# Kernel tuning notes

Hardware: AMD Instinct MI355X
Metric: run time of the kernel (lower is better)

## Reference

```python
import jax, jax.numpy as jnp
import numpy as np

B, T, C = 4, 2048, 1024  # n_embd == input_size == 1024
H, D = 16, 64            # num_heads, head_size


def setup_inputs() -> dict:
    key = jax.random.key(0)
    ks = jax.random.split(key, 5)
    s_in = (1.0 / C) ** 0.5   # ~Linear default init scale
    s_pr = (1.0 / (H * D)) ** 0.5
    return {
        "x": jax.random.normal(ks[0], (B, T, C), dtype=jnp.float32),
        "wq": jax.random.normal(ks[1], (H, C, D), dtype=jnp.float32) * s_in,
        "wk": jax.random.normal(ks[2], (H, C, D), dtype=jnp.float32) * s_in,
        "wv": jax.random.normal(ks[3], (H, C, D), dtype=jnp.float32) * s_in,
        "w_proj": jax.random.normal(ks[4], (H * D, C), dtype=jnp.float32) * s_pr,
        "b_proj": jnp.zeros((C,), dtype=jnp.float32),
    }


def reference(x, wq, wk, wv, w_proj, b_proj):
    Bb, Tt, Cc = x.shape
    # Batched per-head projections: [B,T,C] x [H,C,D] -> [B,H,T,D]
    q = jnp.einsum("btc,hcd->bhtd", x, wq)
    k = jnp.einsum("btc,hcd->bhtd", x, wk)
    v = jnp.einsum("btc,hcd->bhtd", x, wv)
    # NOTE: original scales by C**-0.5 with C = full embedding dim (quirk preserved)
    scale = Cc ** (-0.5)
    scores = jnp.einsum("bhtd,bhsd->bhts", q, k) * scale  # [B,H,T,T]
    causal = jnp.tril(jnp.ones((Tt, Tt), dtype=bool))
    scores = jnp.where(causal, scores, -jnp.inf)
    wei = jax.nn.softmax(scores, axis=-1)
    out = jnp.einsum("bhts,bhsd->bhtd", wei, v)           # [B,H,T,D]
    out = out.transpose(0, 2, 1, 3).reshape(Bb, Tt, -1)    # concat heads [B,T,H*D]
    return out @ w_proj + b_proj                           # [B,T,C]
```

## Files before the change

### kernel.cpp

```cpp
#include <hip/hip_runtime.h>
#include <stdint.h>


typedef uint32_t u32;
typedef __bf16 bf16x8 __attribute__((ext_vector_type(8)));
typedef __bf16 bf16x4 __attribute__((ext_vector_type(4)));
typedef unsigned short us8 __attribute__((ext_vector_type(8)));
typedef float f32x4 __attribute__((ext_vector_type(4)));

#define EXP2F(x) __builtin_amdgcn_exp2f(x)

static __device__ __forceinline__ unsigned short f2bf(float f) {
  union { float f; u32 i; } cv; cv.f = f;
  u32 x = cv.i;
  u32 r = (x + 0x7fffu + ((x >> 16) & 1u)) >> 16;
  return (unsigned short)r;
}

static __device__ __forceinline__ void gload_lds16(const unsigned short* g, unsigned short* l) {
  __builtin_amdgcn_global_load_lds(
      (__attribute__((address_space(1))) u32*)g,
      (__attribute__((address_space(3))) u32*)l, 16, 0, 0);
}

#define G8_LGKM do { asm volatile("s_waitcnt lgkmcnt(0)" ::: "memory"); \
                     __builtin_amdgcn_sched_barrier(0); } while (0)

__global__ __launch_bounds__(256) void prep(
    const float* __restrict__ x, const float* __restrict__ wq,
    const float* __restrict__ wk, const float* __restrict__ wv,
    const float* __restrict__ wp, unsigned short* __restrict__ x_bf,
    unsigned short* __restrict__ wtq, unsigned short* __restrict__ wtp) {
  __shared__ unsigned short lds[64][66];
  const int b = blockIdx.x, tid = threadIdx.x;
  if (b < 4096) {
    size_t i = (size_t)(b * 256 + tid) * 8u;
    float4 a = *(const float4*)(x + i);
    float4 c = *(const float4*)(x + i + 4);
    us8 v;
    v[0] = f2bf(a.x); v[1] = f2bf(a.y); v[2] = f2bf(a.z); v[3] = f2bf(a.w);
    v[4] = f2bf(c.x); v[5] = f2bf(c.y); v[6] = f2bf(c.z); v[7] = f2bf(c.w);
    *(us8*)(x_bf + i) = v;
    return;
  }
  if (b < 4864) {
    int idx = b - 4096;
    int z = idx >> 8, rem = idx & 255;
    int h = rem >> 4, c0 = (rem & 15) << 6;
    const float* src = (z == 0) ? wq : (z == 1) ? wk : wv;
    unsigned short* d = wtq + ((size_t)z << 20);
    const float* s = src + (size_t)h * 65536u + (size_t)c0 * 64u;
#pragma unroll
    for (int it = 0; it < 16; ++it) {
      int i2 = it * 256 + tid;
      int r = i2 >> 6, dd = i2 & 63;
      lds[dd][r] = f2bf(s[r * 64 + dd]);
    }
    __syncthreads();
#pragma unroll
    for (int it = 0; it < 16; ++it) {
      int i2 = it * 256 + tid;
      int dd = i2 >> 6, r = i2 & 63;
      d[(size_t)(h * 64 + dd) * 1024u + c0 + r] = lds[dd][r];
    }
    return;
  }
  {
    int idx = b - 4864;
    int c0 = (idx >> 4) << 6, r0 = (idx & 15) << 6;
#pragma unroll
    for (int it = 0; it < 16; ++it) {
      int i2 = it * 256 + tid;
      int r = i2 >> 6, cc = i2 & 63;
      lds[cc][r] = f2bf(wp[(size_t)(r0 + r) * 1024u + c0 + cc]);
    }
    __syncthreads();
#pragma unroll
    for (int it = 0; it < 16; ++it) {
      int i2 = it * 256 + tid;
      int cc = i2 >> 6, r = i2 & 63;
      wtp[(size_t)(c0 + cc) * 1024u + r0 + r] = lds[cc][r];
    }
  }
}

__global__ __launch_bounds__(256) void transpose_v(
    const unsigned short* __restrict__ v, unsigned short* __restrict__ vt) {
  __shared__ unsigned short lds[64][66];
  const int tid = threadIdx.x;
  const int bh = blockIdx.y, t0 = blockIdx.x * 64;
  const unsigned short* src = v + ((size_t)(bh >> 4) * 2048 + t0) * 1024u + (bh & 15) * 64;
  unsigned short* dst = vt + (size_t)bh * 131072u + t0;
#pragma unroll
  for (int it = 0; it < 16; ++it) {
    int idx = it * 256 + tid;
    int r = idx >> 6, dd = idx & 63;
    lds[dd][r] = src[(size_t)r * 1024u + dd];
  }
  __syncthreads();
#pragma unroll
  for (int it = 0; it < 16; ++it) {
    int idx = it * 256 + tid;
    int dd = idx >> 6, r = idx & 63;
    dst[(size_t)dd * 2048u + r] = lds[dd][r];
  }
}

static __device__ __forceinline__ void gn_stage(const unsigned short* g,
                                                unsigned short* d, int tid) {
#pragma unroll
  for (int l = 0; l < 2; ++l) {
    int cid = l * 512 + tid;
    int r = cid >> 3, c = cid & 7;
    gload_lds16(g + (size_t)r * 1024 + ((c ^ (r & 7)) << 3), d + cid * 8);
  }
}
static __device__ __forceinline__ void gn_ldA(bf16x8 af[4][2], const unsigned short* As,
                                              int wr, int l15, int lhi) {
#pragma unroll
  for (int mi = 0; mi < 4; ++mi)
#pragma unroll
    for (int ks = 0; ks < 2; ++ks) {
      int row = wr * 64 + mi * 16 + l15;
      af[mi][ks] = *(const bf16x8*)(As + row * 64 + ((((ks << 2) | lhi) ^ (row & 7)) << 3));
    }
}
static __device__ __forceinline__ void gn_ldB(bf16x8 bf[2][2], const unsigned short* Bs,
                                              int wc, int np, int l15, int lhi) {
#pragma unroll
  for (int ni = 0; ni < 2; ++ni)
#pragma unroll
    for (int ks = 0; ks < 2; ++ks) {
      int row = wc * 64 + np * 32 + ni * 16 + l15;
      bf[ni][ks] = *(const bf16x8*)(Bs + row * 64 + ((((ks << 2) | lhi) ^ (row & 7)) << 3));
    }
}
static __device__ __forceinline__ void gn_quad(f32x4 acc[4][4], bf16x8 af[4][2],
                                               bf16x8 bf[2][2], int np) {
#pragma unroll
  for (int ks = 0; ks < 2; ++ks)
#pragma unroll
    for (int mi = 0; mi < 4; ++mi)
#pragma unroll
      for (int ni = 0; ni < 2; ++ni)
        acc[mi][np * 2 + ni] = __builtin_amdgcn_mfma_f32_16x16x32_bf16(
            af[mi][ks], bf[ni][ks], acc[mi][np * 2 + ni], 0, 0, 0);
}

template <int F32OUT>
__global__ __launch_bounds__(512, 2) void gemmN(
    const unsigned short* __restrict__ A, const unsigned short* __restrict__ Bt,
    const float* __restrict__ bias, void* __restrict__ Cv) {
  extern __shared__ __align__(16) unsigned short ldsm[];
  unsigned short* Ab = ldsm;
  unsigned short* Bb = ldsm + 16384;
  const int tid = threadIdx.x, wid = tid >> 6, lane = tid & 63;
  const int l15 = lane & 15, lhi = lane >> 4;
  const int wr = wid >> 2, wc = wid & 3;
  const int bid = blockIdx.x;
  const int mt = ((bid & 7) << 3) | ((bid >> 3) & 7);
  const int nt = bid >> 6;
  const int m0 = mt * 128, n0 = nt * 256;
  const unsigned short* Ag = A + (size_t)m0 * 1024;
  const unsigned short* Bg = Bt + (size_t)n0 * 1024;

  f32x4 acc[4][4] = {};
  bf16x8 af[4][2], b0[2][2], b1[2][2];

  gn_stage(Bg, Bb, tid);
  gn_stage(Bg + 128 * 1024, Bb + 8192, tid);
  gn_stage(Ag, Ab, tid);
  gn_stage(Ag + 64, Ab + 8192, tid);
  asm volatile("s_waitcnt vmcnt(2)" ::: "memory");
  __builtin_amdgcn_s_barrier();

  for (int j = 0; j < 8; ++j) {
    const bool last = (j == 7);
    const int kc = j * 128;
    gn_ldA(af, Ab, wr, l15, lhi);
    gn_ldB(b0, Bb, wc, 0, l15, lhi);
    gn_stage(Bg + (kc + 64), Bb + 16384, tid);
    gn_stage(Bg + 128 * 1024 + (kc + 64), Bb + 24576, tid);
    __builtin_amdgcn_s_barrier(); G8_LGKM;
    __builtin_amdgcn_s_setprio(1); gn_quad(acc, af, b0, 0); __builtin_amdgcn_s_setprio(0);
    __builtin_amdgcn_s_barrier();
    gn_ldB(b1, Bb, wc, 1, l15, lhi);
    if (!last) gn_stage(Ag + (kc + 128), Ab, tid);
    __builtin_amdgcn_s_barrier(); G8_LGKM;
    __builtin_amdgcn_s_setprio(1); gn_quad(acc, af, b1, 1); __builtin_amdgcn_s_setprio(0);
    if (last) { asm volatile("s_waitcnt vmcnt(0)" ::: "memory"); }
    else      { asm volatile("s_waitcnt vmcnt(2)" ::: "memory"); }
    __builtin_amdgcn_s_barrier();
    gn_ldA(af, Ab + 8192, wr, l15, lhi);
    gn_ldB(b0, Bb + 16384, wc, 0, l15, lhi);
    if (!last) {
      gn_stage(Bg + (kc + 128), Bb, tid);
      gn_stage(Bg + 128 * 1024 + (kc + 128), Bb + 8192, tid);
    }
    __builtin_amdgcn_s_barrier(); G8_LGKM;
    __builtin_amdgcn_s_setprio(1); gn_quad(acc, af, b0, 0); __builtin_amdgcn_s_setprio(0);
    __builtin_amdgcn_s_barrier();
    gn_ldB(b1, Bb + 16384, wc, 1, l15, lhi);
    if (!last) gn_stage(Ag + (kc + 192), Ab + 8192, tid);
    __builtin_amdgcn_s_barrier(); G8_LGKM;
    __builtin_amdgcn_s_setprio(1); gn_quad(acc, af, b1, 1); __builtin_amdgcn_s_setprio(0);
    if (!last) asm volatile("s_waitcnt vmcnt(2)" ::: "memory");
    __builtin_amdgcn_s_barrier();
  }

#pragma unroll
  for (int mi = 0; mi < 4; ++mi) {
#pragma unroll
    for (int ni = 0; ni < 4; ++ni) {
      const int n = n0 + wc * 64 + ni * 16 + l15;
      const int mr = m0 + wr * 64 + mi * 16 + lhi * 4;
      if constexpr (F32OUT) {
        float* O = (float*)Cv;
        const float b = bias[n];
#pragma unroll
        for (int r = 0; r < 4; ++r)
          O[(size_t)(mr + r) * 1024 + n] = acc[mi][ni][r] + b;
      } else {
        unsigned short* O = (unsigned short*)Cv + ((size_t)(n >> 10) << 23);
        const int nc = n & 1023;
#pragma unroll
        for (int r = 0; r < 4; ++r)
          O[(size_t)(mr + r) * 1024 + nc] = f2bf(acc[mi][ni][r]);
      }
    }
  }
}

#define QT 128
#define KVT 64
#define PSTR 72
#define SCLOG2E 0.04508422f
#define DTHR 128.0f

__global__ __launch_bounds__(512, 4) void attn_fwd(
    const unsigned short* __restrict__ Qg, const unsigned short* __restrict__ Kg,
    const unsigned short* __restrict__ Vtg, unsigned short* __restrict__ Og) {
  __shared__ __align__(16) unsigned short Kl[2][64 * 64];
  __shared__ __align__(16) unsigned short Vl[2][64 * 64];
  __shared__ __align__(16) unsigned short Pl[8][16 * PSTR];
  const int tid = threadIdx.x, wid = tid >> 6, lane = tid & 63;
  const int l15 = lane & 15, lhi = lane >> 4, x7 = lane & 7;
  const int bid = blockIdx.x;
  const int sub = bid & 63, pair = bid >> 6;
  const int bh = ((sub & 7) << 3) | (sub >> 3);
  const int qtA = pair, qtB = 15 - pair;
  const int n0 = 2 * (qtA + 1), n1 = 2 * (qtB + 1);
  const int ntot = n0 + n1;
  const size_t base = (size_t)(bh >> 4) * (2048u * 1024u) + (size_t)(bh & 15) * 64u;
  const size_t vtbase = (size_t)bh * 131072u;

  bf16x8 vones;
#pragma unroll
  for (int j = 0; j < 8; ++j) vones[j] = (__bf16)1.0f;

  auto s0_of = [&](int g) { return ((g < n0) ? g : g - n0) * KVT; };

  auto stage = [&](int bufi, int s0) {
    int q = tid;
    int r = q >> 3;
    int c = (q & 7) ^ (r & 7);
    gload_lds16(Kg + base + (size_t)(s0 + r) * 1024u + c * 8, &Kl[bufi][q * 8]);
    gload_lds16(Vtg + vtbase + (size_t)r * 2048u + s0 + c * 8, &Vl[bufi][q * 8]);
  };

  stage(0, 0);
  __syncthreads();

  int g = 0;
  for (int pass = 0; pass < 2; ++pass) {
    const int qt = pass ? qtB : qtA;
    const int nt = pass ? n1 : n0;
    const int qrow0 = qt * QT + wid * 16;

    bf16x8 qf[2];
#pragma unroll
    for (int kj = 0; kj < 2; ++kj)
      qf[kj] = *(const bf16x8*)(Qg + base +
          (size_t)(qrow0 + l15) * 1024u + kj * 32 + lhi * 8);

    float mrun = -1e30f;
    f32x4 oacc[4] = {};
    f32x4 lacc = {};

    for (int kt = 0; kt < nt; ++kt, ++g) {
      const int cur = g & 1;
      const int s0 = kt * KVT;
      if (g + 1 < ntot) stage(cur ^ 1, s0_of(g + 1));
      if (s0 <= qrow0 + 15) {
        const bool notfull = (s0 + KVT - 1 > qrow0);
        const unsigned short* Kb = Kl[cur];
        const unsigned short* Vb = Vl[cur];

        f32x4 sacc[4] = {};
#pragma unroll
        for (int kj = 0; kj < 2; ++kj) {
          bf16x8 kf[4];
#pragma unroll
          for (int sj = 0; sj < 4; ++sj) {
            int r = sj * 16 + l15;
            kf[sj] = *(const bf16x8*)(&Kb[r * 64 + (((kj * 4 + lhi) ^ x7) * 8)]);
          }
#pragma unroll
          for (int sj = 0; sj < 4; ++sj)
            sacc[sj] = __builtin_amdgcn_mfma_f32_16x16x32_bf16(
                kf[sj], qf[kj], sacc[sj], 0, 0, 0);
        }

        const int qa = qrow0 + l15;
        float mx;
        if (notfull) {
          mx = -3e38f;
#pragma unroll
          for (int sj = 0; sj < 4; ++sj)
#pragma unroll
            for (int r = 0; r < 4; ++r) {
              int sa = s0 + sj * 16 + lhi * 4 + r;
              float v = (sa <= qa) ? sacc[sj][r] : -3e38f;
              sacc[sj][r] = v;
              mx = fmaxf(mx, v);
            }
        } else {
          float m0a = fmaxf(fmaxf(sacc[0][0], sacc[0][1]), fmaxf(sacc[0][2], sacc[0][3]));
          float m1a = fmaxf(fmaxf(sacc[1][0], sacc[1][1]), fmaxf(sacc[1][2], sacc[1][3]));
          float m2a = fmaxf(fmaxf(sacc[2][0], sacc[2][1]), fmaxf(sacc[2][2], sacc[2][3]));
          float m3a = fmaxf(fmaxf(sacc[3][0], sacc[3][1]), fmaxf(sacc[3][2], sacc[3][3]));
          mx = fmaxf(fmaxf(m0a, m1a), fmaxf(m2a, m3a));
        }
        mx = fmaxf(mx, __shfl_xor(mx, 16, 64));
        mx = fmaxf(mx, __shfl_xor(mx, 32, 64));

        if (__any(mx > mrun + DTHR)) {
          float mnew = fmaxf(mrun, mx);
          float sc = EXP2F((mrun - mnew) * SCLOG2E);
          mrun = mnew;
#pragma unroll
          for (int r = 0; r < 4; ++r) {
            float so = __shfl(sc, (lane & 48) + lhi * 4 + r, 64);
#pragma unroll
            for (int dj = 0; dj < 4; ++dj) oacc[dj][r] *= so;
            lacc[r] *= so;
          }
        }

        {
          const float negmC = -mrun * SCLOG2E;
#pragma unroll
          for (int sj = 0; sj < 4; ++sj) {
            float p0 = EXP2F(__builtin_fmaf(sacc[sj][0], SCLOG2E, negmC));
            float p1 = EXP2F(__builtin_fmaf(sacc[sj][1], SCLOG2E, negmC));
            float p2 = EXP2F(__builtin_fmaf(sacc[sj][2], SCLOG2E, negmC));
            float p3 = EXP2F(__builtin_fmaf(sacc[sj][3], SCLOG2E, negmC));
            bf16x4 pk;
            pk[0] = (__bf16)p0; pk[1] = (__bf16)p1;
            pk[2] = (__bf16)p2; pk[3] = (__bf16)p3;
            *(bf16x4*)(&Pl[wid][l15 * PSTR + sj * 16 + lhi * 4]) = pk;
          }
        }

#pragma unroll
        for (int kk = 0; kk < 2; ++kk) {
          bf16x8 pf, vf[4];
          pf = *(const bf16x8*)(&Pl[wid][l15 * PSTR + kk * 32 + lhi * 8]);
#pragma unroll
          for (int dj = 0; dj < 4; ++dj) {
            int r = dj * 16 + l15;
            vf[dj] = *(const bf16x8*)(&Vb[r * 64 + (((kk * 4 + lhi) ^ x7) * 8)]);
          }
#pragma unroll
          for (int dj = 0; dj < 4; ++dj)
            oacc[dj] = __builtin_amdgcn_mfma_f32_16x16x32_bf16(
                pf, vf[dj], oacc[dj], 0, 0, 0);
          lacc = __builtin_amdgcn_mfma_f32_16x16x32_bf16(pf, vones, lacc, 0, 0, 0);
        }
      }

      __syncthreads();
    }

    float rn[4];
#pragma unroll
    for (int r = 0; r < 4; ++r) rn[r] = 1.0f / lacc[r];
#pragma unroll
    for (int dj = 0; dj < 4; ++dj)
#pragma unroll
      for (int r = 0; r < 4; ++r) {
        int t = qrow0 + lhi * 4 + r;
        Og[base + (size_t)t * 1024u + dj * 16 + l15] = f2bf(oacc[dj][r] * rn[r]);
      }
  }
}

extern "C" void kernel_launch(void* const* d_in, const int* in_sizes, int n_in,
                              void* d_out, int out_size, void* d_ws, size_t ws_size,
                              hipStream_t stream) {
  const float* x  = (const float*)d_in[0];
  const float* wq = (const float*)d_in[1];
  const float* wk = (const float*)d_in[2];
  const float* wv = (const float*)d_in[3];
  const float* wp = (const float*)d_in[4];
  const float* bp = (const float*)d_in[5];
  float* out = (float*)d_out;

  unsigned short* ws   = (unsigned short*)d_ws;
  unsigned short* x_bf = ws;
  unsigned short* wtq  = ws + ((size_t)8 << 20);
  unsigned short* wtp  = ws + ((size_t)11 << 20);
  unsigned short* qkv  = ws + ((size_t)12 << 20);
  unsigned short* q    = qkv;
  unsigned short* kk   = qkv + ((size_t)8 << 20);
  unsigned short* vv   = qkv + ((size_t)16 << 20);
  unsigned short* att  = vv;
  unsigned short* vt   = ws + ((size_t)36 << 20);

  (void)hipFuncSetAttribute(reinterpret_cast<const void*>(&gemmN<0>),
                            hipFuncAttributeMaxDynamicSharedMemorySize, 98304);
  (void)hipFuncSetAttribute(reinterpret_cast<const void*>(&gemmN<1>),
                            hipFuncAttributeMaxDynamicSharedMemorySize, 98304);

  prep<<<5120, 256, 0, stream>>>(x, wq, wk, wv, wp, x_bf, wtq, wtp);
  gemmN<0><<<768, 512, 98304, stream>>>(x_bf, wtq, nullptr, qkv);
  transpose_v<<<dim3(32, 64), 256, 0, stream>>>(vv, vt);
  attn_fwd<<<512, 512, 0, stream>>>(q, kk, vt, att);
  gemmN<1><<<256, 512, 98304, stream>>>(att, wtp, bp, out);
}
```

Before: 165.7 us.

## Give each attention wave 32 query rows to reuse K/V fragments

Shrinks the attention block from 8 to 4 waves and has each wave process two 16-row query fragments. Each K and V fragment read from LDS now feeds twice as many MFMAs, and each thread stages two chunks per tile. This cuts LDS read traffic per FLOP. The cost is more registers per wave, fewer waves per block, and coarser causal skipping, since a wave now only skips a tile when both fragments are past the diagonal.

```diff
diff --git a/kernel.cpp b/kernel.cpp
--- a/kernel.cpp
+++ b/kernel.cpp
@@ -237,12 +237,12 @@
 #define SCLOG2E 0.04508422f
 #define DTHR 128.0f
 
-__global__ __launch_bounds__(512, 4) void attn_fwd(
+__global__ __launch_bounds__(256, 2) void attn_fwd(
     const unsigned short* __restrict__ Qg, const unsigned short* __restrict__ Kg,
     const unsigned short* __restrict__ Vtg, unsigned short* __restrict__ Og) {
   __shared__ __align__(16) unsigned short Kl[2][64 * 64];
   __shared__ __align__(16) unsigned short Vl[2][64 * 64];
-  __shared__ __align__(16) unsigned short Pl[8][16 * PSTR];
+  __shared__ __align__(16) unsigned short Pl[4][32 * PSTR];
   const int tid = threadIdx.x, wid = tid >> 6, lane = tid & 63;
   const int l15 = lane & 15, lhi = lane >> 4, x7 = lane & 7;
   const int bid = blockIdx.x;
@@ -261,11 +261,14 @@
   auto s0_of = [&](int g) { return ((g < n0) ? g : g - n0) * KVT; };
 
   auto stage = [&](int bufi, int s0) {
-    int q = tid;
-    int r = q >> 3;
-    int c = (q & 7) ^ (r & 7);
-    gload_lds16(Kg + base + (size_t)(s0 + r) * 1024u + c * 8, &Kl[bufi][q * 8]);
-    gload_lds16(Vtg + vtbase + (size_t)r * 2048u + s0 + c * 8, &Vl[bufi][q * 8]);
+#pragma unroll
+    for (int j = 0; j < 2; ++j) {
+      int q = tid + j * 256;
+      int r = q >> 3;
+      int c = (q & 7) ^ (r & 7);
+      gload_lds16(Kg + base + (size_t)(s0 + r) * 1024u + c * 8, &Kl[bufi][q * 8]);
+      gload_lds16(Vtg + vtbase + (size_t)r * 2048u + s0 + c * 8, &Vl[bufi][q * 8]);
+    }
   };
 
   stage(0, 0);
@@ -275,28 +278,30 @@
   for (int pass = 0; pass < 2; ++pass) {
     const int qt = pass ? qtB : qtA;
     const int nt = pass ? n1 : n0;
-    const int qrow0 = qt * QT + wid * 16;
-
-    bf16x8 qf[2];
-#pragma unroll
-    for (int kj = 0; kj < 2; ++kj)
-      qf[kj] = *(const bf16x8*)(Qg + base +
-          (size_t)(qrow0 + l15) * 1024u + kj * 32 + lhi * 8);
-
-    float mrun = -1e30f;
-    f32x4 oacc[4] = {};
-    f32x4 lacc = {};
+    const int qrow0 = qt * QT + wid * 32;
+
+    bf16x8 qf[2][2];
+#pragma unroll
+    for (int fi = 0; fi < 2; ++fi)
+#pragma unroll
+      for (int kj = 0; kj < 2; ++kj)
+        qf[fi][kj] = *(const bf16x8*)(Qg + base +
+            (size_t)(qrow0 + fi * 16 + l15) * 1024u + kj * 32 + lhi * 8);
+
+    float mrun[2] = {-1e30f, -1e30f};
+    f32x4 oacc[2][4] = {};
+    f32x4 lacc[2] = {};
 
     for (int kt = 0; kt < nt; ++kt, ++g) {
       const int cur = g & 1;
       const int s0 = kt * KVT;
       if (g + 1 < ntot) stage(cur ^ 1, s0_of(g + 1));
-      if (s0 <= qrow0 + 15) {
+      if (s0 <= qrow0 + 31) {
         const bool notfull = (s0 + KVT - 1 > qrow0);
         const unsigned short* Kb = Kl[cur];
         const unsigned short* Vb = Vl[cur];
 
-        f32x4 sacc[4] = {};
+        f32x4 sacc[2][4] = {};
 #pragma unroll
         for (int kj = 0; kj < 2; ++kj) {
           bf16x8 kf[4];
@@ -306,92 +311,114 @@
             kf[sj] = *(const bf16x8*)(&Kb[r * 64 + (((kj * 4 + lhi) ^ x7) * 8)]);
           }
 #pragma unroll
-          for (int sj = 0; sj < 4; ++sj)
-            sacc[sj] = __builtin_amdgcn_mfma_f32_16x16x32_bf16(
-                kf[sj], qf[kj], sacc[sj], 0, 0, 0);
-        }
-
-        const int qa = qrow0 + l15;
-        float mx;
-        if (notfull) {
-          mx = -3e38f;
-#pragma unroll
-          for (int sj = 0; sj < 4; ++sj)
+          for (int fi = 0; fi < 2; ++fi)
+#pragma unroll
+            for (int sj = 0; sj < 4; ++sj)
+              sacc[fi][sj] = __builtin_amdgcn_mfma_f32_16x16x32_bf16(
+                  kf[sj], qf[fi][kj], sacc[fi][sj], 0, 0, 0);
+        }
+
+        float mx[2];
+#pragma unroll
+        for (int fi = 0; fi < 2; ++fi) {
+          const int qa = qrow0 + fi * 16 + l15;
+          if (notfull) {
+            float m = -3e38f;
+#pragma unroll
+            for (int sj = 0; sj < 4; ++sj)
+#pragma unroll
+              for (int r = 0; r < 4; ++r) {
+                int sa = s0 + sj * 16 + lhi * 4 + r;
+                float v = (sa <= qa) ? sacc[fi][sj][r] : -3e38f;
+                sacc[fi][sj][r] = v;
+                m = fmaxf(m, v);
+              }
+            mx[fi] = m;
+          } else {
+            float m0a = fmaxf(fmaxf(sacc[fi][0][0], sacc[fi][0][1]), fmaxf(sacc[fi][0][2], sacc[fi][0][3]));
+            float m1a = fmaxf(fmaxf(sacc[fi][1][0], sacc[fi][1][1]), fmaxf(sacc[fi][1][2], sacc[fi][1][3]));
+            float m2a = fmaxf(fmaxf(sacc[fi][2][0], sacc[fi][2][1]), fmaxf(sacc[fi][2][2], sacc[fi][2][3]));
+            float m3a = fmaxf(fmaxf(sacc[fi][3][0], sacc[fi][3][1]), fmaxf(sacc[fi][3][2], sacc[fi][3][3]));
+            mx[fi] = fmaxf(fmaxf(m0a, m1a), fmaxf(m2a, m3a));
+          }
+          mx[fi] = fmaxf(mx[fi], __shfl_xor(mx[fi], 16, 64));
+          mx[fi] = fmaxf(mx[fi], __shfl_xor(mx[fi], 32, 64));
+        }
+
+        bool needR = (mx[0] > mrun[0] + DTHR) || (mx[1] > mrun[1] + DTHR);
+        if (__any(needR)) {
+          float sc[2];
+#pragma unroll
+          for (int fi = 0; fi < 2; ++fi) {
+            float mnew = fmaxf(mrun[fi], mx[fi]);
+            sc[fi] = EXP2F((mrun[fi] - mnew) * SCLOG2E);
+            mrun[fi] = mnew;
+          }
+#pragma unroll
+          for (int fi = 0; fi < 2; ++fi)
 #pragma unroll
             for (int r = 0; r < 4; ++r) {
-              int sa = s0 + sj * 16 + lhi * 4 + r;
-              float v = (sa <= qa) ? sacc[sj][r] : -3e38f;
-              sacc[sj][r] = v;
-              mx = fmaxf(mx, v);
+              float so = __shfl(sc[fi], (lane & 48) + lhi * 4 + r, 64);
+#pragma unroll
+              for (int dj = 0; dj < 4; ++dj) oacc[fi][dj][r] *= so;
+              lacc[fi][r] *= so;
             }
-        } else {
-          float m0a = fmaxf(fmaxf(sacc[0][0], sacc[0][1]), fmaxf(sacc[0][2], sacc[0][3]));
-          float m1a = fmaxf(fmaxf(sacc[1][0], sacc[1][1]), fmaxf(sacc[1][2], sacc[1][3]));
-          float m2a = fmaxf(fmaxf(sacc[2][0], sacc[2][1]), fmaxf(sacc[2][2], sacc[2][3]));
-          float m3a = fmaxf(fmaxf(sacc[3][0], sacc[3][1]), fmaxf(sacc[3][2], sacc[3][3]));
-          mx = fmaxf(fmaxf(m0a, m1a), fmaxf(m2a, m3a));
-        }
-        mx = fmaxf(mx, __shfl_xor(mx, 16, 64));
-        mx = fmaxf(mx, __shfl_xor(mx, 32, 64));
-
-        if (__any(mx > mrun + DTHR)) {
-          float mnew = fmaxf(mrun, mx);
-          float sc = EXP2F((mrun - mnew) * SCLOG2E);
-          mrun = mnew;
-#pragma unroll
-          for (int r = 0; r < 4; ++r) {
-            float so = __shfl(sc, (lane & 48) + lhi * 4 + r, 64);
-#pragma unroll
-            for (int dj = 0; dj < 4; ++dj) oacc[dj][r] *= so;
-            lacc[r] *= so;
-          }
-        }
-
-        {
-          const float negmC = -mrun * SCLOG2E;
+        }
+
+#pragma unroll
+        for (int fi = 0; fi < 2; ++fi) {
+          const float negmC = -mrun[fi] * SCLOG2E;
 #pragma unroll
           for (int sj = 0; sj < 4; ++sj) {
-            float p0 = EXP2F(__builtin_fmaf(sacc[sj][0], SCLOG2E, negmC));
-            float p1 = EXP2F(__builtin_fmaf(sacc[sj][1], SCLOG2E, negmC));
-            float p2 = EXP2F(__builtin_fmaf(sacc[sj][2], SCLOG2E, negmC));
-            float p3 = EXP2F(__builtin_fmaf(sacc[sj][3], SCLOG2E, negmC));
+            float p0 = EXP2F(__builtin_fmaf(sacc[fi][sj][0], SCLOG2E, negmC));
+            float p1 = EXP2F(__builtin_fmaf(sacc[fi][sj][1], SCLOG2E, negmC));
+            float p2 = EXP2F(__builtin_fmaf(sacc[fi][sj][2], SCLOG2E, negmC));
+            float p3 = EXP2F(__builtin_fmaf(sacc[fi][sj][3], SCLOG2E, negmC));
             bf16x4 pk;
             pk[0] = (__bf16)p0; pk[1] = (__bf16)p1;
             pk[2] = (__bf16)p2; pk[3] = (__bf16)p3;
-            *(bf16x4*)(&Pl[wid][l15 * PSTR + sj * 16 + lhi * 4]) = pk;
+            *(bf16x4*)(&Pl[wid][(fi * 16 + l15) * PSTR + sj * 16 + lhi * 4]) = pk;
           }
         }
 
 #pragma unroll
         for (int kk = 0; kk < 2; ++kk) {
-          bf16x8 pf, vf[4];
-          pf = *(const bf16x8*)(&Pl[wid][l15 * PSTR + kk * 32 + lhi * 8]);
+          bf16x8 pf[2], vf[4];
+#pragma unroll
+          for (int fi = 0; fi < 2; ++fi)
+            pf[fi] = *(const bf16x8*)(&Pl[wid][(fi * 16 + l15) * PSTR + kk * 32 + lhi * 8]);
 #pragma unroll
           for (int dj = 0; dj < 4; ++dj) {
             int r = dj * 16 + l15;
             vf[dj] = *(const bf16x8*)(&Vb[r * 64 + (((kk * 4 + lhi) ^ x7) * 8)]);
           }
 #pragma unroll
-          for (int dj = 0; dj < 4; ++dj)
-            oacc[dj] = __builtin_amdgcn_mfma_f32_16x16x32_bf16(
-                pf, vf[dj], oacc[dj], 0, 0, 0);
-          lacc = __builtin_amdgcn_mfma_f32_16x16x32_bf16(pf, vones, lacc, 0, 0, 0);
+          for (int fi = 0; fi < 2; ++fi) {
+#pragma unroll
+            for (int dj = 0; dj < 4; ++dj)
+              oacc[fi][dj] = __builtin_amdgcn_mfma_f32_16x16x32_bf16(
+                  pf[fi], vf[dj], oacc[fi][dj], 0, 0, 0);
+            lacc[fi] = __builtin_amdgcn_mfma_f32_16x16x32_bf16(pf[fi], vones, lacc[fi], 0, 0, 0);
+          }
         }
       }
 
       __syncthreads();
     }
 
-    float rn[4];
-#pragma unroll
-    for (int r = 0; r < 4; ++r) rn[r] = 1.0f / lacc[r];
-#pragma unroll
-    for (int dj = 0; dj < 4; ++dj)
-#pragma unroll
-      for (int r = 0; r < 4; ++r) {
-        int t = qrow0 + lhi * 4 + r;
-        Og[base + (size_t)t * 1024u + dj * 16 + l15] = f2bf(oacc[dj][r] * rn[r]);
-      }
+#pragma unroll
+    for (int fi = 0; fi < 2; ++fi) {
+      float rn[4];
+#pragma unroll
+      for (int r = 0; r < 4; ++r) rn[r] = 1.0f / lacc[fi][r];
+#pragma unroll
+      for (int dj = 0; dj < 4; ++dj)
+#pragma unroll
+        for (int r = 0; r < 4; ++r) {
+          int t = qrow0 + fi * 16 + lhi * 4 + r;
+          Og[base + (size_t)t * 1024u + dj * 16 + l15] = f2bf(oacc[fi][dj][r] * rn[r]);
+        }
+    }
   }
 }
 
@@ -425,6 +452,6 @@
   prep<<<5120, 256, 0, stream>>>(x, wq, wk, wv, wp, x_bf, wtq, wtp);
   gemmN<0><<<768, 512, 98304, stream>>>(x_bf, wtq, nullptr, qkv);
   transpose_v<<<dim3(32, 64), 256, 0, stream>>>(vv, vt);
-  attn_fwd<<<512, 512, 0, stream>>>(q, kk, vt, att);
+  attn_fwd<<<512, 256, 0, stream>>>(q, kk, vt, att);
   gemmN<1><<<256, 512, 98304, stream>>>(att, wtp, bp, out);
 }
```

After: 167.0 us. Within noise of the previous version (+0.8%).
